# Performance work log

Measured on AMD Instinct MI355X. Metric: run time of the kernel, lower is better.

The kernel has to match this reference:

```python
import jax, jax.numpy as jnp
import numpy as np

# --- static config (matches init_kwargs) ---
B, N, FD, Y, X = 2, 4, 128, 64, 64   # batch, n_views, feat_dim, H, W
DIM, HEADS, DH = 128, 4, 128          # dim, heads, dim_head (= dim)
INNER = HEADS * DH                    # 512
BN = B * N
EPS = 1e-5


def _ln(x, g, b):
    # LayerNorm over last dim, eps=1e-5, affine
    m = x.mean(-1, keepdims=True)
    v = ((x - m) ** 2).mean(-1, keepdims=True)
    return (x - m) * jax.lax.rsqrt(v + EPS) * g + b


def _inorm(x):
    # InstanceNorm2d (no affine): normalize each (sample, channel) over H,W
    m = x.mean((2, 3), keepdims=True)
    v = ((x - m) ** 2).mean((2, 3), keepdims=True)
    return (x - m) * jax.lax.rsqrt(v + EPS)


def _conv2x2_s2(x, w):
    # Conv2d(k=2, stride=2, no bias): non-overlapping windows -> einsum
    b, c, h, wd = x.shape
    xp = x.reshape(b, c, h // 2, 2, wd // 2, 2)
    return jnp.einsum('bchawd,ocad->bohw', xp, w)


def _convT2x2_s2(x, w):
    # ConvTranspose2d(k=2, stride=2, no bias); w in torch layout (I, O, 2, 2)
    b, i, h, wd = x.shape
    y = jnp.einsum('bihw,ioad->bohawd', x, w)
    return y.reshape(b, w.shape[1], 2 * h, 2 * wd)


def _forward(cam_feat, lidar_feat, pos_embed, conv_w, convT_w,
             lnq_g, lnq_b, wq, lnk_g, lnk_b, wk, lnv_g, lnv_b, wv,
             proj_w, proj_b, pre_g, pre_b,
             mlp_w1, mlp_b1, mlp_w2, mlp_b2, post_g, post_b):
    h, w = Y // 2, X // 2
    bev = pos_embed[None, None]                      # (1,1,FD,Y,X)
    cam = (cam_feat + bev).reshape(BN, FD, Y, X)
    lid = (lidar_feat + bev).reshape(BN, FD, Y, X)
    cam_e = _conv2x2_s2(jax.nn.relu(_inorm(cam)), conv_w)   # (BN,DIM,h,w)
    lid_e = _conv2x2_s2(jax.nn.relu(_inorm(lid)), conv_w)

    cam_flat = cam_e.reshape(BN, DIM, h * w)
    lid_flat = lid_e.reshape(BN, DIM, h * w)
    # query = cat([cam, lidar]) along token axis -> (BN, 2hw, DIM)
    q_in = jnp.concatenate([cam_flat, lid_flat], -1).transpose(0, 2, 1)
    # skip = cat([cam_embed, lidar_embed]) along width -> 'b d H W -> b (H W) d'
    skip = jnp.concatenate([cam_e, lid_e], -1).transpose(0, 2, 3, 1).reshape(BN, 2 * h * w, DIM)

    def cross(kv_flat):
        k_in = kv_flat.transpose(0, 2, 1)            # (BN, hw, DIM)
        q = (_ln(q_in, lnq_g, lnq_b) @ wq).reshape(BN, -1, HEADS, DH)
        k = (_ln(k_in, lnk_g, lnk_b) @ wk).reshape(BN, -1, HEADS, DH)
        v = (_ln(k_in, lnv_g, lnv_b) @ wv).reshape(BN, -1, HEADS, DH)
        dot = jnp.einsum('bqhd,bkhd->bhqk', q, k) * (DH ** -0.5)
        att = jax.nn.softmax(dot, axis=-1)
        a = jnp.einsum('bhqk,bkhd->bqhd', att, v).reshape(BN, -1, INNER)
        z = a @ proj_w + proj_b + skip
        z = _ln(z, pre_g, pre_b)
        z = z + (jax.nn.gelu(z @ mlp_w1 + mlp_b1, approximate=False) @ mlp_w2 + mlp_b2)
        z = _ln(z, post_g, post_b)
        # '(b l) (H W) d -> b l d H W' with H=Y, W=X//2
        return z.reshape(B, N, Y, X // 2, DIM).transpose(0, 1, 4, 2, 3)

    cam_fused = cross(cam_flat)                      # (B,N,DIM,Y,X//2)
    lid_fused = cross(lid_flat)
    fused = cam_fused + lid_fused
    # 'b l d (m h) w -> b l d h w m' then sum over m=2
    fused = fused.reshape(B, N, DIM, 2, Y // 2, X // 2).sum(3)
    fused_feat = _convT2x2_s2(jax.nn.relu(_inorm(fused.reshape(BN, DIM, Y // 2, X // 2))), convT_w)
    cam_out = _convT2x2_s2(jax.nn.relu(_inorm(cam_fused.reshape(BN, DIM, Y, X // 2))), convT_w)
    lid_out = _convT2x2_s2(jax.nn.relu(_inorm(lid_fused.reshape(BN, DIM, Y, X // 2))), convT_w)
    return fused_feat, cam_out, lid_out


def setup_inputs() -> dict:
    key = jax.random.key(0)
    ks = jax.random.split(key, 12)
    f = lambda k, shape, s=0.02: (jax.random.normal(k, shape, jnp.float32) * s)
    return {
        'cam_feat': jax.random.normal(ks[0], (B, N, FD, Y, X), jnp.float32),
        'lidar_feat': jax.random.normal(ks[1], (B, N, FD, Y, X), jnp.float32),
        'pos_embed': jax.random.normal(ks[2], (FD, Y, X), jnp.float32),
        'conv_w': f(ks[3], (DIM, FD, 2, 2), 0.05),
        'convT_w': f(ks[4], (DIM, FD, 2, 2), 0.05),
        'lnq_g': jnp.ones(DIM), 'lnq_b': jnp.zeros(DIM), 'wq': f(ks[5], (DIM, INNER)),
        'lnk_g': jnp.ones(DIM), 'lnk_b': jnp.zeros(DIM), 'wk': f(ks[6], (DIM, INNER)),
        'lnv_g': jnp.ones(DIM), 'lnv_b': jnp.zeros(DIM), 'wv': f(ks[7], (DIM, INNER)),
        'proj_w': f(ks[8], (INNER, DIM)), 'proj_b': jnp.zeros(DIM),
        'pre_g': jnp.ones(DIM), 'pre_b': jnp.zeros(DIM),
        'mlp_w1': f(ks[9], (DIM, 2 * DIM)), 'mlp_b1': jnp.zeros(2 * DIM),
        'mlp_w2': f(ks[10], (2 * DIM, DIM)), 'mlp_b2': jnp.zeros(DIM),
        'post_g': jnp.ones(DIM), 'post_b': jnp.zeros(DIM),
    }


def reference(cam_feat, lidar_feat, pos_embed, conv_w, convT_w,
              lnq_g, lnq_b, wq, lnk_g, lnk_b, wk, lnv_g, lnv_b, wv,
              proj_w, proj_b, pre_g, pre_b,
              mlp_w1, mlp_b1, mlp_w2, mlp_b2, post_g, post_b):
    return _forward(cam_feat, lidar_feat, pos_embed, conv_w, convT_w,
                    lnq_g, lnq_b, wq, lnk_g, lnk_b, wk, lnv_g, lnv_b, wv,
                    proj_w, proj_b, pre_g, pre_b,
                    mlp_w1, mlp_b1, mlp_w2, mlp_b2, post_g, post_b)
```

## Files before the change

kernel.cpp:

```cpp
#include <hip/hip_runtime.h>
#include <math.h>

#define TPB 256

typedef __attribute__((ext_vector_type(8))) short bf16x8;
typedef __attribute__((ext_vector_type(4))) float f32x4;

__device__ __forceinline__ float gelu_exact(float x) {
    return 0.5f * x * (1.0f + erff(x * 0.70710678118654752f));
}

__device__ __forceinline__ unsigned short f2bf(float x) {
    unsigned u = __float_as_uint(x);
    return (unsigned short)((u + 0x7fffu + ((u >> 16) & 1u)) >> 16);
}

__global__ void k_stats_cm(const float* __restrict__ x0, const float* __restrict__ x1,
                           const float* __restrict__ pos, float* __restrict__ mean,
                           float* __restrict__ rstd) {
    int gc = blockIdx.x;
    const float* src = ((gc < 1024) ? x0 : x1) + (size_t)(gc & 1023) * 4096;
    const float* posr = pos + (size_t)(gc & 127) * 4096;
    float s = 0.f, s2 = 0.f;
    for (int p = threadIdx.x; p < 4096; p += TPB) {
        float v = src[p] + posr[p];
        s += v; s2 += v * v;
    }
#pragma unroll
    for (int m = 32; m; m >>= 1) { s += __shfl_xor(s, m); s2 += __shfl_xor(s2, m); }
    __shared__ float ls[4], ls2[4];
    int w = threadIdx.x >> 6;
    if ((threadIdx.x & 63) == 0) { ls[w] = s; ls2[w] = s2; }
    __syncthreads();
    if (threadIdx.x == 0) {
        s = ls[0] + ls[1] + ls[2] + ls[3];
        s2 = ls2[0] + ls2[1] + ls2[2] + ls2[3];
        float mu = s / 4096.f;
        float var = s2 / 4096.f - mu * mu;
        mean[gc] = mu;
        rstd[gc] = rsqrtf(var + 1e-5f);
    }
}

__global__ void k_stats_red(const float* __restrict__ part, float* __restrict__ mean,
                            float* __restrict__ rstd, int nc, int T) {
    int b = blockIdx.x, d = threadIdx.x;
    float s = 0.f, s2 = 0.f;
    for (int c = 0; c < nc; c++) {
        const float* p = part + ((size_t)(b * nc + c) * 2) * 128;
        s += p[d]; s2 += p[128 + d];
    }
    float mu = s / (float)T;
    float var = s2 / (float)T - mu * mu;
    mean[b * 128 + d] = mu;
    rstd[b * 128 + d] = rsqrtf(var + 1e-5f);
}

__global__ void k_stats_red2(const float* __restrict__ part,
                             float* __restrict__ meanC, float* __restrict__ rstdC,
                             float* __restrict__ meanL, float* __restrict__ rstdL) {
    int idx = blockIdx.x, d = threadIdx.x;
    int sel = idx >> 3, b = idx & 7;
    float s = 0.f, s2 = 0.f;
    for (int c = 0; c < 32; c++) {
        const float* p = part + ((size_t)((sel * 8 + b) * 32 + c) * 2) * 128;
        s += p[d]; s2 += p[128 + d];
    }
    float mu = s / 2048.f;
    float var = s2 / 2048.f - mu * mu;
    float* mean = sel ? meanL : meanC;
    float* rstd = sel ? rstdL : rstdC;
    mean[b * 128 + d] = mu;
    rstd[b * 128 + d] = rsqrtf(var + 1e-5f);
}

__global__ void k_prep(const float* __restrict__ cam, const float* __restrict__ lid,
                       const float* __restrict__ pos, const float* __restrict__ mean,
                       const float* __restrict__ rstd, unsigned short* __restrict__ xcolT) {
    __shared__ unsigned short T[32 * 520];
    int h = blockIdx.x, bb = blockIdx.y;
    int b = bb & 7, so = (bb < 8) ? 0 : 1024;
    const float* x = (bb < 8) ? cam : lid;
    int tid = threadIdx.x;
    for (int i = tid; i < 4096; i += TPB) {
        int c = i >> 5, w = i & 31;
        int ch = b * 128 + c;
        const float* xr = x + (size_t)ch * 4096 + (2 * h) * 64 + 2 * w;
        const float* pr = pos + (size_t)c * 4096 + (2 * h) * 64 + 2 * w;
        float mu = mean[so + ch], rs = rstd[so + ch];
        float2 x0 = *(const float2*)xr;
        float2 x1 = *(const float2*)(xr + 64);
        float2 p0 = *(const float2*)pr;
        float2 p1 = *(const float2*)(pr + 64);
        ushort4 u;
        u.x = f2bf(fmaxf((x0.x + p0.x - mu) * rs, 0.f));
        u.y = f2bf(fmaxf((x0.y + p0.y - mu) * rs, 0.f));
        u.z = f2bf(fmaxf((x1.x + p1.x - mu) * rs, 0.f));
        u.w = f2bf(fmaxf((x1.y + p1.y - mu) * rs, 0.f));
        *(ushort4*)&T[w * 520 + c * 4] = u;
    }
    __syncthreads();
    unsigned short* dst = xcolT + ((size_t)bb * 1024 + h * 32) * 512;
    for (int i = tid; i < 2048; i += TPB) {
        int w = i >> 6, kk = (i & 63) * 8;
        *(bf16x8*)&dst[(size_t)w * 512 + kk] = *(bf16x8*)&T[w * 520 + kk];
    }
}

__global__ __launch_bounds__(256, 2) void k_conv_gemm(
        const float* __restrict__ W, const unsigned short* __restrict__ xcolT,
        float* __restrict__ camT, float* __restrict__ lidT,
        float* __restrict__ mean_e, float* __restrict__ rstd_e) {
    __shared__ __align__(16) unsigned short As[128 * 40];
    __shared__ __align__(16) unsigned short Bs[64 * 40];
    __shared__ float red[2048];
    int tid = threadIdx.x, lane = tid & 63, w = tid >> 6;
    int l16 = lane & 15, lhi = lane >> 4;
    int n0 = blockIdx.x * 64, bb = blockIdx.z;
    const unsigned short* BT = xcolT + (size_t)bb * 524288;
    float* eT = ((bb < 8) ? camT : lidT) + (size_t)(bb & 7) * 131072;

    f32x4 acc[2][4];
#pragma unroll
    for (int mi = 0; mi < 2; mi++)
#pragma unroll
        for (int ni = 0; ni < 4; ni++) acc[mi][ni] = (f32x4){0.f, 0.f, 0.f, 0.f};

    for (int k0 = 0; k0 < 512; k0 += 32) {
        for (int i = tid; i < 1024; i += TPB) {
            int row = i >> 3, kc = (i & 7) * 4;
            float4 va = *(const float4*)&W[(size_t)row * 512 + k0 + kc];
            ushort4 u;
            u.x = f2bf(va.x); u.y = f2bf(va.y); u.z = f2bf(va.z); u.w = f2bf(va.w);
            *(ushort4*)&As[row * 40 + kc] = u;
        }
        for (int i = tid; i < 256; i += TPB) {
            int n = i >> 2, kc = (i & 3) * 8;
            *(bf16x8*)&Bs[n * 40 + kc] = *(const bf16x8*)&BT[(size_t)(n0 + n) * 512 + k0 + kc];
        }
        __syncthreads();
        bf16x8 af[2], bfr[4];
#pragma unroll
        for (int mi = 0; mi < 2; mi++)
            af[mi] = *(bf16x8*)&As[(w * 32 + mi * 16 + l16) * 40 + lhi * 8];
#pragma unroll
        for (int ni = 0; ni < 4; ni++)
            bfr[ni] = *(bf16x8*)&Bs[(ni * 16 + l16) * 40 + lhi * 8];
#pragma unroll
        for (int mi = 0; mi < 2; mi++)
#pragma unroll
            for (int ni = 0; ni < 4; ni++)
                acc[mi][ni] = __builtin_amdgcn_mfma_f32_16x16x32_bf16(af[mi], bfr[ni], acc[mi][ni], 0, 0, 0);
        __syncthreads();
    }
#pragma unroll
    for (int mi = 0; mi < 2; mi++)
#pragma unroll
        for (int ni = 0; ni < 4; ni++) {
            int col = n0 + ni * 16 + l16;
            int rowb = w * 32 + mi * 16 + lhi * 4;
            *(float4*)&eT[(size_t)col * 128 + rowb] = *(float4*)&acc[mi][ni];
        }
#pragma unroll
    for (int ni = 0; ni < 4; ni++) {
        float s = 0.f, s2 = 0.f;
#pragma unroll
        for (int mi = 0; mi < 2; mi++)
#pragma unroll
            for (int rg = 0; rg < 4; rg++) {
                float v = acc[mi][ni][rg];
                s += v; s2 += v * v;
            }
        int idx = (ni * 16 + l16) * 16 + w * 4 + lhi;
        red[idx] = s;
        red[1024 + idx] = s2;
    }
    __syncthreads();
    if (tid < 64) {
        int ni = tid >> 4, c16 = tid & 15;
        float s = 0.f, s2 = 0.f;
#pragma unroll
        for (int j = 0; j < 16; j++) {
            s += red[(ni * 16 + c16) * 16 + j];
            s2 += red[1024 + (ni * 16 + c16) * 16 + j];
        }
        int col = n0 + ni * 16 + c16;
        int tok = bb * 1024 + col;
        float mu = s * (1.f / 128.f);
        float var = s2 * (1.f / 128.f) - mu * mu;
        mean_e[tok] = mu;
        rstd_e[tok] = rsqrtf(var + 1e-5f);
    }
}

__global__ void k_wtrans_all(
        const float* __restrict__ wq, const float* __restrict__ wk,
        const float* __restrict__ wv, const float* __restrict__ proj,
        const float* __restrict__ m1, const float* __restrict__ m2,
        const float* __restrict__ ct,
        const float* __restrict__ gq, const float* __restrict__ gk,
        const float* __restrict__ gv,
        const float* __restrict__ bq_in, const float* __restrict__ bk_in,
        const float* __restrict__ bv_in,
        unsigned short* wqT, unsigned short* wkT, unsigned short* wvT,
        unsigned short* projT, unsigned short* m1T, unsigned short* m2T,
        unsigned short* ctT, float* __restrict__ bout) {
    __shared__ float t[32][33];
    int bid = blockIdx.x;
    int tid = threadIdx.x;
    if (bid >= 384) {
        int i = bid - 384;
        int which = i >> 1, half = i & 1;
        const float* W = (which == 0) ? wq : (which == 1) ? wk : wv;
        const float* bb = (which == 0) ? bq_in : (which == 1) ? bk_in : bv_in;
        int n = half * 256 + tid;
        float s = 0.f;
        for (int k = 0; k < 128; k++) s += bb[k] * W[(size_t)k * 512 + n];
        bout[which * 512 + n] = s;
        return;
    }
    const float* W; unsigned short* WT; const float* sc = nullptr; int K, N, ti;
    if (bid < 64)       { W = wq;   WT = wqT;   sc = gq; K = 128; N = 512; ti = bid; }
    else if (bid < 128) { W = wk;   WT = wkT;   sc = gk; K = 128; N = 512; ti = bid - 64; }
    else if (bid < 192) { W = wv;   WT = wvT;   sc = gv; K = 128; N = 512; ti = bid - 128; }
    else if (bid < 256) { W = proj; WT = projT; K = 512; N = 128; ti = bid - 192; }
    else if (bid < 288) { W = m1;   WT = m1T;   K = 128; N = 256; ti = bid - 256; }
    else if (bid < 320) { W = m2;   WT = m2T;   K = 256; N = 128; ti = bid - 288; }
    else                { W = ct;   WT = ctT;   K = 128; N = 512; ti = bid - 320; }
    int tx = N >> 5;
    int n0 = (ti % tx) * 32, k0 = (ti / tx) * 32;
    for (int i = tid; i < 1024; i += TPB) {
        int r = i >> 5, c = i & 31;
        float v = W[(size_t)(k0 + r) * N + n0 + c];
        if (sc) v *= sc[k0 + r];
        t[r][c] = v;
    }
    __syncthreads();
    for (int i = tid; i < 1024; i += TPB) {
        int r = i >> 5, c = i & 31;
        WT[(size_t)(n0 + r) * K + k0 + c] = f2bf(t[c][r]);
    }
}

__global__ __launch_bounds__(256, 2) void k_qkv_gemm(
        const float* __restrict__ camT, const float* __restrict__ lidT,
        const float* __restrict__ me, const float* __restrict__ re,
        const unsigned short* __restrict__ wqT, const unsigned short* __restrict__ wkT,
        const unsigned short* __restrict__ wvT,
        unsigned short* __restrict__ qout, unsigned short* __restrict__ kout,
        unsigned short* __restrict__ vout,
        const float* __restrict__ bvecs, float qscale) {
    __shared__ __align__(16) unsigned short As[128 * 40];
    __shared__ __align__(16) unsigned short Bs[128 * 40];
    int tid = threadIdx.x, lane = tid & 63, w = tid >> 6;
    int l16 = lane & 15, lhi = lane >> 4;
    int wm = w >> 1, wn = w & 1;
    int which = blockIdx.x >> 2;
    int n0 = (blockIdx.x & 3) * 128;
    int m0 = blockIdx.y * 128;
    const unsigned short* BT = (which == 0) ? wqT : (which == 1) ? wkT : wvT;
    const float* bias = bvecs + which * 512;

    f32x4 acc[4][4];
#pragma unroll
    for (int mi = 0; mi < 4; mi++)
#pragma unroll
        for (int ni = 0; ni < 4; ni++) acc[mi][ni] = (f32x4){0.f, 0.f, 0.f, 0.f};

    for (int k0 = 0; k0 < 128; k0 += 32) {
        for (int i = tid; i < 1024; i += TPB) {
            int row = i >> 3, kc = (i & 7) * 4;
            int r = m0 + row;
            const float* srow;
            int tok;
            if (which == 0) {
                int b = r >> 11, t = r & 2047;
                bool cam = t < 1024;
                tok = (cam ? b : 8 + b) * 1024 + (t & 1023);
                srow = (cam ? camT : lidT) + (size_t)(b * 1024 + (t & 1023)) * 128;
            } else {
                tok = r;
                srow = ((r < 8192) ? camT : lidT) + (size_t)(r & 8191) * 128;
            }
            float mu = me[tok], rs = re[tok];
            float4 va = *(const float4*)&srow[k0 + kc];
            ushort4 u;
            u.x = f2bf((va.x - mu) * rs); u.y = f2bf((va.y - mu) * rs);
            u.z = f2bf((va.z - mu) * rs); u.w = f2bf((va.w - mu) * rs);
            *(ushort4*)&As[row * 40 + kc] = u;
        }
        for (int i = tid; i < 512; i += TPB) {
            int n = i >> 2, kc = (i & 3) * 8;
            *(bf16x8*)&Bs[n * 40 + kc] = *(const bf16x8*)&BT[(size_t)(n0 + n) * 128 + k0 + kc];
        }
        __syncthreads();
        bf16x8 af[4], bfr[4];
#pragma unroll
        for (int mi = 0; mi < 4; mi++)
            af[mi] = *(bf16x8*)&As[(wm * 64 + mi * 16 + l16) * 40 + lhi * 8];
#pragma unroll
        for (int ni = 0; ni < 4; ni++)
            bfr[ni] = *(bf16x8*)&Bs[(wn * 64 + ni * 16 + l16) * 40 + lhi * 8];
#pragma unroll
        for (int mi = 0; mi < 4; mi++)
#pragma unroll
            for (int ni = 0; ni < 4; ni++)
                acc[mi][ni] = __builtin_amdgcn_mfma_f32_16x16x32_bf16(af[mi], bfr[ni], acc[mi][ni], 0, 0, 0);
        __syncthreads();
    }
#pragma unroll
    for (int mi = 0; mi < 4; mi++) {
#pragma unroll
        for (int ni = 0; ni < 4; ni++) {
            int col = n0 + wn * 64 + ni * 16 + l16;
            float bc = bias[col];
            if (which == 2) {
                int row0 = m0 + wm * 64 + mi * 16 + lhi * 4;
                int bb = row0 >> 10, t0 = row0 & 1023;
                ushort4 u;
                u.x = f2bf(acc[mi][ni][0] + bc); u.y = f2bf(acc[mi][ni][1] + bc);
                u.z = f2bf(acc[mi][ni][2] + bc); u.w = f2bf(acc[mi][ni][3] + bc);
                *(ushort4*)&vout[(((size_t)(bb * 4 + (col >> 7))) * 128 + (col & 127)) * 1024 + t0] = u;
            } else {
                int sT = (which == 0) ? 11 : 10;
                float sc = (which == 0) ? qscale : 1.f;
                unsigned short* C16 = (which == 0) ? qout : kout;
#pragma unroll
                for (int rg = 0; rg < 4; rg++) {
                    int row = m0 + wm * 64 + mi * 16 + lhi * 4 + rg;
                    int bb = row >> sT, t = row & ((1 << sT) - 1);
                    size_t oa = ((((size_t)bb * 4 + (col >> 7)) << sT) + t) * 128 + (col & 127);
                    C16[oa] = f2bf((acc[mi][ni][rg] + bc) * sc);
                }
            }
        }
    }
}

__global__ __launch_bounds__(256, 2) void k_gemm_gelu(
        const float* __restrict__ A, const unsigned short* __restrict__ BT,
        unsigned short* __restrict__ C16, int N, int K,
        const float* __restrict__ bias) {
    __shared__ __align__(16) unsigned short As[128 * 40];
    __shared__ __align__(16) unsigned short Bs[128 * 40];
    int tid = threadIdx.x, lane = tid & 63, w = tid >> 6;
    int l16 = lane & 15, lhi = lane >> 4;
    int wm = w >> 1, wn = w & 1;
    int m0 = blockIdx.y * 128, n0 = blockIdx.x * 128;

    f32x4 acc[4][4];
#pragma unroll
    for (int mi = 0; mi < 4; mi++)
#pragma unroll
        for (int ni = 0; ni < 4; ni++) acc[mi][ni] = (f32x4){0.f, 0.f, 0.f, 0.f};

    for (int k0 = 0; k0 < K; k0 += 32) {
        for (int i = tid; i < 1024; i += TPB) {
            int row = i >> 3, kc = (i & 7) * 4;
            float4 va = *(const float4*)&A[(size_t)(m0 + row) * K + k0 + kc];
            ushort4 u;
            u.x = f2bf(va.x); u.y = f2bf(va.y); u.z = f2bf(va.z); u.w = f2bf(va.w);
            *(ushort4*)&As[row * 40 + kc] = u;
        }
        for (int i = tid; i < 512; i += TPB) {
            int n = i >> 2, kc = (i & 3) * 8;
            *(bf16x8*)&Bs[n * 40 + kc] = *(const bf16x8*)&BT[(size_t)(n0 + n) * K + k0 + kc];
        }
        __syncthreads();
        bf16x8 af[4], bfr[4];
#pragma unroll
        for (int mi = 0; mi < 4; mi++)
            af[mi] = *(bf16x8*)&As[(wm * 64 + mi * 16 + l16) * 40 + lhi * 8];
#pragma unroll
        for (int ni = 0; ni < 4; ni++)
            bfr[ni] = *(bf16x8*)&Bs[(wn * 64 + ni * 16 + l16) * 40 + lhi * 8];
#pragma unroll
        for (int mi = 0; mi < 4; mi++)
#pragma unroll
            for (int ni = 0; ni < 4; ni++)
                acc[mi][ni] = __builtin_amdgcn_mfma_f32_16x16x32_bf16(af[mi], bfr[ni], acc[mi][ni], 0, 0, 0);
        __syncthreads();
    }
#pragma unroll
    for (int mi = 0; mi < 4; mi++)
#pragma unroll
        for (int ni = 0; ni < 4; ni++) {
            int col = n0 + wn * 64 + ni * 16 + l16;
            float bc = bias[col];
#pragma unroll
            for (int rg = 0; rg < 4; rg++) {
                int row = m0 + wm * 64 + mi * 16 + lhi * 4 + rg;
                C16[(size_t)row * N + col] = f2bf(gelu_exact(acc[mi][ni][rg] + bc));
            }
        }
}

__global__ __launch_bounds__(256, 2) void k_gemm_ln(
        const unsigned short* __restrict__ Ab, const unsigned short* __restrict__ BT,
        float* __restrict__ C0, float* __restrict__ C1, int K, int mode,
        const float* __restrict__ bias, const float* __restrict__ aux,
        const float* __restrict__ aux2,
        const float* __restrict__ g, const float* __restrict__ bvec,
        float* __restrict__ part) {
    __shared__ __align__(16) char shm[64 * 132 * 4];
    unsigned short* As = (unsigned short*)shm;
    unsigned short* Bs = As + 64 * 40;
    float* Cs = (float*)shm;
    int tid = threadIdx.x, lane = tid & 63, w = tid >> 6;
    int l16 = lane & 15, lhi = lane >> 4;
    int m0 = blockIdx.x * 64;

    f32x4 acc[4][2];
#pragma unroll
    for (int mi = 0; mi < 4; mi++)
#pragma unroll
        for (int ni = 0; ni < 2; ni++) acc[mi][ni] = (f32x4){0.f, 0.f, 0.f, 0.f};

    for (int k0 = 0; k0 < K; k0 += 32) {
        for (int i = tid; i < 256; i += TPB) {
            int row = i >> 2, kc = (i & 3) * 8;
            *(bf16x8*)&As[row * 40 + kc] =
                *(const bf16x8*)&Ab[(size_t)(m0 + row) * K + k0 + kc];
        }
        for (int i = tid; i < 512; i += TPB) {
            int n = i >> 2, kc = (i & 3) * 8;
            *(bf16x8*)&Bs[n * 40 + kc] = *(const bf16x8*)&BT[(size_t)n * K + k0 + kc];
        }
        __syncthreads();
        bf16x8 af[4], bfr[2];
#pragma unroll
        for (int mi = 0; mi < 4; mi++)
            af[mi] = *(bf16x8*)&As[(mi * 16 + l16) * 40 + lhi * 8];
#pragma unroll
        for (int ni = 0; ni < 2; ni++)
            bfr[ni] = *(bf16x8*)&Bs[(w * 32 + ni * 16 + l16) * 40 + lhi * 8];
#pragma unroll
        for (int mi = 0; mi < 4; mi++)
#pragma unroll
            for (int ni = 0; ni < 2; ni++)
                acc[mi][ni] = __builtin_amdgcn_mfma_f32_16x16x32_bf16(af[mi], bfr[ni], acc[mi][ni], 0, 0, 0);
        __syncthreads();
    }
#pragma unroll
    for (int mi = 0; mi < 4; mi++) {
#pragma unroll
        for (int ni = 0; ni < 2; ni++) {
            int col = w * 32 + ni * 16 + l16;
#pragma unroll
            for (int rg = 0; rg < 4; rg++) {
                int rl = mi * 16 + lhi * 4 + rg;
                int grow = m0 + rl;
                float v = acc[mi][ni][rg] + bias[col];
                if (mode == 0) {
                    int rr = grow & 16383;
                    int b = rr >> 11, s = rr & 2047;
                    int H = s >> 6, W = s & 63;
                    const float* sp = (W < 32) ? aux : aux2;
                    v += sp[((size_t)(b * 1024 + H * 32 + (W & 31))) * 128 + col];
                } else {
                    v += aux[(size_t)grow * 128 + col];
                }
                Cs[rl * 132 + col] = v;
            }
        }
    }
    __syncthreads();
    float sl = 0.f, sl2 = 0.f, sh = 0.f, sh2 = 0.f;
    for (int rr = 0; rr < 16; rr++) {
        int row = w * 16 + rr, grow = m0 + row;
        float x0 = Cs[row * 132 + lane], x1 = Cs[row * 132 + 64 + lane];
        float s = x0 + x1, s2 = x0 * x0 + x1 * x1;
#pragma unroll
        for (int m = 32; m; m >>= 1) { s += __shfl_xor(s, m); s2 += __shfl_xor(s2, m); }
        float mu = s * (1.f / 128.f);
        float var = s2 * (1.f / 128.f) - mu * mu;
        float rs = rsqrtf(var + 1e-5f);
        float o0 = (x0 - mu) * rs * g[lane] + bvec[lane];
        float o1 = (x1 - mu) * rs * g[lane + 64] + bvec[lane + 64];
        float* Cp;
        size_t ro;
        if (mode == 1) { Cp = (grow < 16384) ? C0 : C1; ro = (size_t)(grow & 16383) * 128; }
        else           { Cp = C0; ro = (size_t)grow * 128; }
        Cp[ro + lane]      = o0;
        Cp[ro + lane + 64] = o1;
        sl += o0; sl2 += o0 * o0; sh += o1; sh2 += o1 * o1;
    }
    if (mode == 1) {
        __syncthreads();
        float* redS = Cs;
        redS[w * 128 + lane] = sl;
        redS[w * 128 + 64 + lane] = sh;
        redS[512 + w * 128 + lane] = sl2;
        redS[512 + w * 128 + 64 + lane] = sh2;
        __syncthreads();
        if (tid < 128) {
            int d = tid;
            float S = 0.f, S2 = 0.f;
#pragma unroll
            for (int j = 0; j < 4; j++) {
                S += redS[j * 128 + d];
                S2 += redS[512 + j * 128 + d];
            }
            int sel = (m0 >= 16384) ? 1 : 0;
            int rrg = m0 & 16383;
            int b = rrg >> 11, c = (rrg >> 6) & 31;
            float* p = part + ((size_t)((sel * 8 + b) * 32 + c) * 2) * 128;
            p[d] = S; p[128 + d] = S2;
        }
    }
}

__global__ __launch_bounds__(256, 2) void k_convt_gemm(
        const float* __restrict__ srcF, const float* __restrict__ srcC,
        const float* __restrict__ srcL, const float* __restrict__ stats,
        const unsigned short* __restrict__ ctT, float* __restrict__ outp) {
    __shared__ __align__(16) unsigned short As[128 * 40];
    __shared__ __align__(16) unsigned short Bs[128 * 40];
    int tid = threadIdx.x, lane = tid & 63, w = tid >> 6;
    int l16 = lane & 15, lhi = lane >> 4;
    int wm = w >> 1, wn = w & 1;
    int my = blockIdx.y, n0 = blockIdx.x * 128, b = blockIdx.z;
    const float* src; const float* mean; const float* rstd; float* out;
    int M, Hin, m0;
    if (my < 8)       { src = srcF; mean = stats + 4096; rstd = stats + 5120;
                        out = outp;            M = 1024; Hin = 32; m0 = my * 128; }
    else if (my < 24) { src = srcC; mean = stats + 6144; rstd = stats + 7168;
                        out = outp + 4194304;  M = 2048; Hin = 64; m0 = (my - 8) * 128; }
    else              { src = srcL; mean = stats + 8192; rstd = stats + 9216;
                        out = outp + 12582912; M = 2048; Hin = 64; m0 = (my - 24) * 128; }
    const float* Ab = src + (size_t)b * M * 128;
    const float* mb = mean + b * 128;
    const float* rb = rstd + b * 128;

    f32x4 acc[4][4];
#pragma unroll
    for (int mi = 0; mi < 4; mi++)
#pragma unroll
        for (int ni = 0; ni < 4; ni++) acc[mi][ni] = (f32x4){0.f, 0.f, 0.f, 0.f};

    for (int k0 = 0; k0 < 128; k0 += 32) {
        for (int i = tid; i < 1024; i += TPB) {
            int row = i >> 3, kc = (i & 7) * 4;
            float4 va = *(const float4*)&Ab[(size_t)(m0 + row) * 128 + k0 + kc];
            float4 mn = *(const float4*)&mb[k0 + kc];
            float4 rs = *(const float4*)&rb[k0 + kc];
            ushort4 u;
            u.x = f2bf(fmaxf((va.x - mn.x) * rs.x, 0.f));
            u.y = f2bf(fmaxf((va.y - mn.y) * rs.y, 0.f));
            u.z = f2bf(fmaxf((va.z - mn.z) * rs.z, 0.f));
            u.w = f2bf(fmaxf((va.w - mn.w) * rs.w, 0.f));
            *(ushort4*)&As[row * 40 + kc] = u;
        }
        for (int i = tid; i < 512; i += TPB) {
            int n = i >> 2, kc = (i & 3) * 8;
            *(bf16x8*)&Bs[n * 40 + kc] = *(const bf16x8*)&ctT[(size_t)(n0 + n) * 128 + k0 + kc];
        }
        __syncthreads();
        bf16x8 af[4], bfr[4];
#pragma unroll
        for (int mi = 0; mi < 4; mi++)
            af[mi] = *(bf16x8*)&As[(wm * 64 + mi * 16 + l16) * 40 + lhi * 8];
#pragma unroll
        for (int ni = 0; ni < 4; ni++)
            bfr[ni] = *(bf16x8*)&Bs[(wn * 64 + ni * 16 + l16) * 40 + lhi * 8];
#pragma unroll
        for (int mi = 0; mi < 4; mi++)
#pragma unroll
            for (int ni = 0; ni < 4; ni++)
                acc[mi][ni] = __builtin_amdgcn_mfma_f32_16x16x32_bf16(af[mi], bfr[ni], acc[mi][ni], 0, 0, 0);
        __syncthreads();
    }
    int Ho = 2 * Hin, Wo = 64;
#pragma unroll
    for (int mi = 0; mi < 4; mi++) {
#pragma unroll
        for (int ni = 0; ni < 4; ni++) {
            int col = n0 + wn * 64 + ni * 16 + l16;
            int oc = col >> 2, aa = (col >> 1) & 1, dd = col & 1;
            int p0 = m0 + wm * 64 + mi * 16 + lhi * 4;
            int hin = p0 >> 5, win0 = p0 & 31;
            float s0 = __shfl_xor(acc[mi][ni][0], 1);
            float s1 = __shfl_xor(acc[mi][ni][1], 1);
            float s2 = __shfl_xor(acc[mi][ni][2], 1);
            float s3 = __shfl_xor(acc[mi][ni][3], 1);
            float4 o;
            if (!dd) o = make_float4(acc[mi][ni][0], s0, acc[mi][ni][1], s1);
            else     o = make_float4(s2, acc[mi][ni][2], s3, acc[mi][ni][3]);
            size_t addr = (((size_t)b * 128 + oc) * Ho + 2 * hin + aa) * Wo
                        + 2 * win0 + (dd ? 4 : 0);
            *(float4*)&out[addr] = o;
        }
    }
}

__global__ __launch_bounds__(256, 2) void k_attn_bf16(
        const unsigned short* __restrict__ qb, const unsigned short* __restrict__ kb,
        const unsigned short* __restrict__ vt, unsigned short* __restrict__ aout) {
    __shared__ __align__(16) unsigned short smem[24576];
    unsigned short* Ks = smem;
    unsigned short* Vt = smem + 8192;
    unsigned short* Ps = smem + 16384;
    int tid = threadIdx.x;
    int lane = tid & 63, w = tid >> 6;
    int l16 = lane & 15, lhi = lane >> 4;
    int bid = blockIdx.x;
    int xcd = bid & 7, j = bid >> 3;
    int hz = xcd * 8 + (j >> 4);
    int qt = j & 15;
    int h = hz & 3, z = hz >> 2;
    int bh_q = (z & 7) * 4 + h;
    int bh_kv = z * 4 + h;
    unsigned short* Pw = Ps + w * 2048;

    const unsigned short* qg = qb + ((size_t)bh_q * 2048 + qt * 128) * 128;
    bf16x8 qa[2][4];
#pragma unroll
    for (int mt = 0; mt < 2; mt++) {
        int r = w * 32 + mt * 16 + l16;
#pragma unroll
        for (int ks = 0; ks < 4; ks++)
            qa[mt][ks] = *(const bf16x8*)&qg[(size_t)r * 128 + ks * 32 + lhi * 8];
    }

    f32x4 acc[2][8];
#pragma unroll
    for (int mt = 0; mt < 2; mt++)
#pragma unroll
        for (int dt = 0; dt < 8; dt++) acc[mt][dt] = (f32x4){0.f, 0.f, 0.f, 0.f};
    float m_r[2] = {-1e30f, -1e30f};
    float l_r[2] = {0.f, 0.f};

    const unsigned short* kg = kb + (size_t)bh_kv * 131072;
    const unsigned short* vg = vt + (size_t)bh_kv * 131072;

    int krow = tid >> 4, kcol = (tid & 15) * 8;
    int kls = ((tid & 15) ^ (krow & 7)) << 3;
    int vrow = tid >> 3, vcol = (tid & 7) * 8;
    int vls = ((tid & 7) ^ (vrow & 7)) << 3;

#pragma unroll
    for (int jj = 0; jj < 4; jj++) {
        int r = krow + jj * 16;
        *(bf16x8*)&Ks[r * 128 + kls] = *(const bf16x8*)&kg[(size_t)r * 128 + kcol];
        int d = vrow + jj * 32;
        *(bf16x8*)&Vt[d * 64 + vls] = *(const bf16x8*)&vg[(size_t)d * 1024 + vcol];
    }
    __syncthreads();

    for (int c = 0; c < 16; c++) {
        bf16x8 kpre[4], vpre[4];
        if (c < 15) {
            int c0 = (c + 1) * 64;
#pragma unroll
            for (int jj = 0; jj < 4; jj++) {
                kpre[jj] = *(const bf16x8*)&kg[(size_t)(c0 + krow + jj * 16) * 128 + kcol];
                vpre[jj] = *(const bf16x8*)&vg[(size_t)(vrow + jj * 32) * 1024 + c0 + vcol];
            }
        }

        f32x4 s[2][4];
#pragma unroll
        for (int mt = 0; mt < 2; mt++)
#pragma unroll
            for (int kt = 0; kt < 4; kt++) s[mt][kt] = (f32x4){0.f, 0.f, 0.f, 0.f};
        __builtin_amdgcn_s_setprio(1);
#pragma unroll
        for (int kt = 0; kt < 4; kt++) {
            int r = kt * 16 + l16;
#pragma unroll
            for (int ks = 0; ks < 4; ks++) {
                bf16x8 kf = *(bf16x8*)&Ks[r * 128 + (((ks * 4 + lhi) ^ (r & 7)) << 3)];
                s[0][kt] = __builtin_amdgcn_mfma_f32_16x16x32_bf16(kf, qa[0][ks], s[0][kt], 0, 0, 0);
                s[1][kt] = __builtin_amdgcn_mfma_f32_16x16x32_bf16(kf, qa[1][ks], s[1][kt], 0, 0, 0);
            }
        }
        __builtin_amdgcn_s_setprio(0);

        float pm[2];
#pragma unroll
        for (int mt = 0; mt < 2; mt++) {
            float a = s[mt][0][0];
#pragma unroll
            for (int kt = 0; kt < 4; kt++)
#pragma unroll
                for (int rg = 0; rg < 4; rg++) a = fmaxf(a, s[mt][kt][rg]);
            a = fmaxf(a, __shfl_xor(a, 16));
            a = fmaxf(a, __shfl_xor(a, 32));
            pm[mt] = a;
        }
        bool need = (pm[0] > m_r[0] + 8.f) || (pm[1] > m_r[1] + 8.f);
        if (__any(need)) {
#pragma unroll
            for (int mt = 0; mt < 2; mt++) {
                float mn = fmaxf(m_r[mt], pm[mt]);
                float f = __builtin_amdgcn_exp2f(m_r[mt] - mn);
                m_r[mt] = mn;
                l_r[mt] *= f;
#pragma unroll
                for (int rg = 0; rg < 4; rg++) {
                    float ft = __shfl(f, lhi * 4 + rg);
#pragma unroll
                    for (int dt = 0; dt < 8; dt++) acc[mt][dt][rg] *= ft;
                }
            }
        }

#pragma unroll
        for (int mt = 0; mt < 2; mt++) {
            int row = mt * 16 + l16;
            int rsw = row & 7;
            float ls = 0.f;
#pragma unroll
            for (int kt = 0; kt < 4; kt++) {
                float p0 = __builtin_amdgcn_exp2f(s[mt][kt][0] - m_r[mt]);
                float p1 = __builtin_amdgcn_exp2f(s[mt][kt][1] - m_r[mt]);
                float p2 = __builtin_amdgcn_exp2f(s[mt][kt][2] - m_r[mt]);
                float p3 = __builtin_amdgcn_exp2f(s[mt][kt][3] - m_r[mt]);
                ls += (p0 + p1) + (p2 + p3);
                unsigned u01, u23;
                asm("v_cvt_pk_bf16_f32 %0, %1, %2" : "=v"(u01) : "v"(p0), "v"(p1));
                asm("v_cvt_pk_bf16_f32 %0, %1, %2" : "=v"(u23) : "v"(p2), "v"(p3));
                int slot = kt * 2 + (lhi >> 1);
                int base = row * 64 + ((slot ^ rsw) << 3) + (lhi & 1) * 4;
                *(unsigned*)&Pw[base] = u01;
                *(unsigned*)&Pw[base + 2] = u23;
            }
            l_r[mt] += ls;
        }
        asm volatile("s_waitcnt lgkmcnt(0)" ::: "memory");

        bf16x8 pa0[2], pa1[2];
#pragma unroll
        for (int mt = 0; mt < 2; mt++) {
            int row = mt * 16 + l16;
            pa0[mt] = *(bf16x8*)&Pw[row * 64 + ((lhi ^ (row & 7)) << 3)];
            pa1[mt] = *(bf16x8*)&Pw[row * 64 + (((4 + lhi) ^ (row & 7)) << 3)];
        }
        __builtin_amdgcn_s_setprio(1);
#pragma unroll
        for (int dt = 0; dt < 8; dt++) {
            int d = dt * 16 + l16;
            bf16x8 vb0 = *(bf16x8*)&Vt[d * 64 + ((lhi ^ (d & 7)) << 3)];
            bf16x8 vb1 = *(bf16x8*)&Vt[d * 64 + (((4 + lhi) ^ (d & 7)) << 3)];
            acc[0][dt] = __builtin_amdgcn_mfma_f32_16x16x32_bf16(pa0[0], vb0, acc[0][dt], 0, 0, 0);
            acc[0][dt] = __builtin_amdgcn_mfma_f32_16x16x32_bf16(pa1[0], vb1, acc[0][dt], 0, 0, 0);
            acc[1][dt] = __builtin_amdgcn_mfma_f32_16x16x32_bf16(pa0[1], vb0, acc[1][dt], 0, 0, 0);
            acc[1][dt] = __builtin_amdgcn_mfma_f32_16x16x32_bf16(pa1[1], vb1, acc[1][dt], 0, 0, 0);
        }
        __builtin_amdgcn_s_setprio(0);
        __syncthreads();

        if (c < 15) {
#pragma unroll
            for (int jj = 0; jj < 4; jj++) {
                *(bf16x8*)&Ks[(krow + jj * 16) * 128 + kls] = kpre[jj];
                *(bf16x8*)&Vt[(vrow + jj * 32) * 64 + vls] = vpre[jj];
            }
            __syncthreads();
        }
    }

#pragma unroll
    for (int mt = 0; mt < 2; mt++) {
        float lt = l_r[mt];
        lt += __shfl_xor(lt, 16);
        lt += __shfl_xor(lt, 32);
        l_r[mt] = lt;
    }
    size_t obase = (size_t)(z >> 3) * 16384 + (size_t)(z & 7) * 2048;
#pragma unroll
    for (int mt = 0; mt < 2; mt++)
#pragma unroll
        for (int rg = 0; rg < 4; rg++) {
            float linv = 1.f / __shfl(l_r[mt], lhi * 4 + rg);
            int qrow = qt * 128 + w * 32 + mt * 16 + lhi * 4 + rg;
            unsigned short* orow = aout + (obase + qrow) * 512 + h * 128;
#pragma unroll
            for (int dt = 0; dt < 8; dt++)
                orow[dt * 16 + l16] = f2bf(acc[mt][dt][rg] * linv);
        }
}

__global__ void k_fused_stats(const float* __restrict__ zc, const float* __restrict__ zl,
                              float* __restrict__ fs, float* __restrict__ part) {
    int c = blockIdx.x, b = blockIdx.y;
    int tid = threadIdx.x;
    int d = tid & 127, half = tid >> 7;
    size_t base0 = ((size_t)b * 2048 + c * 64) * 128;
    size_t base1 = ((size_t)b * 2048 + 1024 + c * 64) * 128;
    float s = 0.f, s2 = 0.f;
    for (int t = half; t < 64; t += 2) {
        float v = zc[base0 + t * 128 + d] + zc[base1 + t * 128 + d]
                + zl[base0 + t * 128 + d] + zl[base1 + t * 128 + d];
        fs[((size_t)b * 1024 + c * 64 + t) * 128 + d] = v;
        s += v; s2 += v * v;
    }
    __shared__ float ls[256], ls2[256];
    ls[tid] = s; ls2[tid] = s2;
    __syncthreads();
    if (tid < 128) {
        s = ls[tid] + ls[tid + 128];
        s2 = ls2[tid] + ls2[tid + 128];
        float* p = part + ((size_t)(b * 16 + c) * 2) * 128;
        p[d] = s; p[128 + d] = s2;
    }
}

extern "C" void kernel_launch(void* const* d_in, const int* in_sizes, int n_in,
                              void* d_out, int out_size, void* d_ws, size_t ws_size,
                              hipStream_t stream) {
    const float* cam_feat = (const float*)d_in[0];
    const float* lid_feat = (const float*)d_in[1];
    const float* pos      = (const float*)d_in[2];
    const float* conv_w   = (const float*)d_in[3];
    const float* convT_w  = (const float*)d_in[4];
    const float* lnq_g = (const float*)d_in[5];
    const float* lnq_b = (const float*)d_in[6];
    const float* wq    = (const float*)d_in[7];
    const float* lnk_g = (const float*)d_in[8];
    const float* lnk_b = (const float*)d_in[9];
    const float* wk    = (const float*)d_in[10];
    const float* lnv_g = (const float*)d_in[11];
    const float* lnv_b = (const float*)d_in[12];
    const float* wv    = (const float*)d_in[13];
    const float* proj_w = (const float*)d_in[14];
    const float* proj_b = (const float*)d_in[15];
    const float* pre_g = (const float*)d_in[16];
    const float* pre_b = (const float*)d_in[17];
    const float* mlp_w1 = (const float*)d_in[18];
    const float* mlp_b1 = (const float*)d_in[19];
    const float* mlp_w2 = (const float*)d_in[20];
    const float* mlp_b2 = (const float*)d_in[21];
    const float* post_g = (const float*)d_in[22];
    const float* post_b = (const float*)d_in[23];

    float* ws = (float*)d_ws;
    float* outp = (float*)d_out;

    float* cam_eT  = ws + 0;
    float* lid_eT  = ws + 1048576;
    unsigned short* qbf16 = (unsigned short*)(ws + 2097152);
    float* z_cam   = ws + 6291456;
    float* z_lid   = ws + 8388608;
    float* fused_s = ws + 10485760;
    float* stats   = ws + 11534336;
    unsigned short* wbuf = (unsigned short*)(ws + 11550720);
    float* part    = ws + 11747328;
    float* mean_e  = ws + 11878400;
    float* rstd_e  = ws + 11894784;
    float* bvecs   = ws + 11911168;
    unsigned short* xcolT = (unsigned short*)(ws + 11912704);
    float* pool    = ws + 16107008;

    unsigned short* wqT   = wbuf + 0;
    unsigned short* wkT   = wbuf + 65536;
    unsigned short* wvT   = wbuf + 131072;
    unsigned short* projT = wbuf + 196608;
    unsigned short* m1T   = wbuf + 262144;
    unsigned short* m2T   = wbuf + 294912;
    unsigned short* ctT   = wbuf + 327680;

    float* meanA = stats + 0,    *rstdA = stats + 2048;
    float* meanF = stats + 4096, *rstdF = stats + 5120;

    unsigned short* kbf16 = (unsigned short*)(pool + 0);
    unsigned short* vbfT  = (unsigned short*)(pool + 4194304);
    unsigned short* abuf  = (unsigned short*)(pool + 8388608);
    float* z2 = pool + 0;
    unsigned short* h1 = (unsigned short*)(pool + 4194304);

    const float qscale = 0.12751744436f;

    k_wtrans_all<<<390, TPB, 0, stream>>>(wq, wk, wv, proj_w, mlp_w1, mlp_w2, convT_w,
                                          lnq_g, lnk_g, lnv_g, lnq_b, lnk_b, lnv_b,
                                          wqT, wkT, wvT, projT, m1T, m2T, ctT, bvecs);

    k_stats_cm<<<2048, TPB, 0, stream>>>(cam_feat, lid_feat, pos, meanA, rstdA);
    k_prep<<<dim3(32, 16), TPB, 0, stream>>>(cam_feat, lid_feat, pos, meanA, rstdA, xcolT);
    k_conv_gemm<<<dim3(16, 1, 16), TPB, 0, stream>>>(conv_w, xcolT, cam_eT, lid_eT,
                                                     mean_e, rstd_e);

    k_qkv_gemm<<<dim3(12, 128), TPB, 0, stream>>>(
        cam_eT, lid_eT, mean_e, rstd_e, wqT, wkT, wvT, qbf16, kbf16, vbfT,
        bvecs, qscale);
    k_attn_bf16<<<1024, TPB, 0, stream>>>(qbf16, kbf16, vbfT, abuf);
    k_gemm_ln<<<512, TPB, 0, stream>>>(
        abuf, projT, z2, nullptr, 512, 0, proj_b, cam_eT, lid_eT, pre_g, pre_b, nullptr);
    k_gemm_gelu<<<dim3(2, 256), TPB, 0, stream>>>(z2, m1T, h1, 256, 128, mlp_b1);
    k_gemm_ln<<<512, TPB, 0, stream>>>(
        h1, m2T, z_cam, z_lid, 256, 1, mlp_b2, z2, nullptr, post_g, post_b, part);

    k_stats_red2<<<16, 128, 0, stream>>>(part, stats + 6144, stats + 7168,
                                         stats + 8192, stats + 9216);
    k_fused_stats<<<dim3(16, 8), TPB, 0, stream>>>(z_cam, z_lid, fused_s, part + 65536);
    k_stats_red<<<8, 128, 0, stream>>>(part + 65536, meanF, rstdF, 16, 1024);
    k_convt_gemm<<<dim3(4, 40, 8), TPB, 0, stream>>>(fused_s, z_cam, z_lid, stats,
                                                     ctT, outp);
}
```

Measured before the change: 298.2 us.

## Fuse projection, pre-LN, MLP and post-LN into one per-token-tile kernel

Replaces three kernels (proj GEMM+LN, MLP1 GEMM+GELU, MLP2 GEMM+LN) with a single kernel that keeps each 64-token tile's intermediates in registers and swizzled LDS. Computing the transposed product lets each lane own one token's full row, so LayerNorm needs only a few shuffles. This removes the global round-trips for z2 and h1 and two launches. In exchange the MLP weights are re-streamed per block and register pressure is higher, which may reduce occupancy.

```diff
diff --git a/kernel.cpp b/kernel.cpp
--- a/kernel.cpp
+++ b/kernel.cpp
@@ -337,176 +337,203 @@
     }
 }
 
-__global__ __launch_bounds__(256, 2) void k_gemm_gelu(
-        const float* __restrict__ A, const unsigned short* __restrict__ BT,
-        unsigned short* __restrict__ C16, int N, int K,
-        const float* __restrict__ bias) {
-    __shared__ __align__(16) unsigned short As[128 * 40];
-    __shared__ __align__(16) unsigned short Bs[128 * 40];
-    int tid = threadIdx.x, lane = tid & 63, w = tid >> 6;
-    int l16 = lane & 15, lhi = lane >> 4;
-    int wm = w >> 1, wn = w & 1;
-    int m0 = blockIdx.y * 128, n0 = blockIdx.x * 128;
-
-    f32x4 acc[4][4];
-#pragma unroll
-    for (int mi = 0; mi < 4; mi++)
-#pragma unroll
-        for (int ni = 0; ni < 4; ni++) acc[mi][ni] = (f32x4){0.f, 0.f, 0.f, 0.f};
-
-    for (int k0 = 0; k0 < K; k0 += 32) {
-        for (int i = tid; i < 1024; i += TPB) {
-            int row = i >> 3, kc = (i & 7) * 4;
-            float4 va = *(const float4*)&A[(size_t)(m0 + row) * K + k0 + kc];
-            ushort4 u;
-            u.x = f2bf(va.x); u.y = f2bf(va.y); u.z = f2bf(va.z); u.w = f2bf(va.w);
-            *(ushort4*)&As[row * 40 + kc] = u;
-        }
-        for (int i = tid; i < 512; i += TPB) {
-            int n = i >> 2, kc = (i & 3) * 8;
-            *(bf16x8*)&Bs[n * 40 + kc] = *(const bf16x8*)&BT[(size_t)(n0 + n) * K + k0 + kc];
-        }
-        __syncthreads();
-        bf16x8 af[4], bfr[4];
-#pragma unroll
-        for (int mi = 0; mi < 4; mi++)
-            af[mi] = *(bf16x8*)&As[(wm * 64 + mi * 16 + l16) * 40 + lhi * 8];
-#pragma unroll
-        for (int ni = 0; ni < 4; ni++)
-            bfr[ni] = *(bf16x8*)&Bs[(wn * 64 + ni * 16 + l16) * 40 + lhi * 8];
-#pragma unroll
-        for (int mi = 0; mi < 4; mi++)
-#pragma unroll
-            for (int ni = 0; ni < 4; ni++)
-                acc[mi][ni] = __builtin_amdgcn_mfma_f32_16x16x32_bf16(af[mi], bfr[ni], acc[mi][ni], 0, 0, 0);
-        __syncthreads();
-    }
-#pragma unroll
-    for (int mi = 0; mi < 4; mi++)
-#pragma unroll
-        for (int ni = 0; ni < 4; ni++) {
-            int col = n0 + wn * 64 + ni * 16 + l16;
-            float bc = bias[col];
-#pragma unroll
-            for (int rg = 0; rg < 4; rg++) {
-                int row = m0 + wm * 64 + mi * 16 + lhi * 4 + rg;
-                C16[(size_t)row * N + col] = f2bf(gelu_exact(acc[mi][ni][rg] + bc));
-            }
-        }
-}
-
-__global__ __launch_bounds__(256, 2) void k_gemm_ln(
-        const unsigned short* __restrict__ Ab, const unsigned short* __restrict__ BT,
-        float* __restrict__ C0, float* __restrict__ C1, int K, int mode,
-        const float* __restrict__ bias, const float* __restrict__ aux,
-        const float* __restrict__ aux2,
-        const float* __restrict__ g, const float* __restrict__ bvec,
+__global__ __launch_bounds__(256, 2) void k_tail_fused(
+        const unsigned short* __restrict__ abuf, const unsigned short* __restrict__ projT,
+        const unsigned short* __restrict__ m1T, const unsigned short* __restrict__ m2T,
+        const float* __restrict__ camT, const float* __restrict__ lidT,
+        const float* __restrict__ proj_b,
+        const float* __restrict__ pre_g, const float* __restrict__ pre_b,
+        const float* __restrict__ mlp_b1, const float* __restrict__ mlp_b2,
+        const float* __restrict__ post_g, const float* __restrict__ post_b,
+        float* __restrict__ z_cam, float* __restrict__ z_lid,
         float* __restrict__ part) {
-    __shared__ __align__(16) char shm[64 * 132 * 4];
-    unsigned short* As = (unsigned short*)shm;
-    unsigned short* Bs = As + 64 * 40;
-    float* Cs = (float*)shm;
+    __shared__ __align__(16) unsigned short shm[21504];
     int tid = threadIdx.x, lane = tid & 63, w = tid >> 6;
     int l16 = lane & 15, lhi = lane >> 4;
     int m0 = blockIdx.x * 64;
-
-    f32x4 acc[4][2];
-#pragma unroll
-    for (int mi = 0; mi < 4; mi++)
-#pragma unroll
-        for (int ni = 0; ni < 2; ni++) acc[mi][ni] = (f32x4){0.f, 0.f, 0.f, 0.f};
-
-    for (int k0 = 0; k0 < K; k0 += 32) {
+    int tok = w * 16 + l16;
+    int grow = m0 + tok;
+    int tsw = tok & 7;
+
+    unsigned short* Ts = shm;
+    unsigned short* Ws = shm + 2560;
+    f32x4 z2[8];
+#pragma unroll
+    for (int ni = 0; ni < 8; ni++) z2[ni] = (f32x4){0.f, 0.f, 0.f, 0.f};
+    for (int k0 = 0; k0 < 512; k0 += 32) {
         for (int i = tid; i < 256; i += TPB) {
             int row = i >> 2, kc = (i & 3) * 8;
-            *(bf16x8*)&As[row * 40 + kc] =
-                *(const bf16x8*)&Ab[(size_t)(m0 + row) * K + k0 + kc];
+            *(bf16x8*)&Ts[row * 40 + kc] =
+                *(const bf16x8*)&abuf[(size_t)(m0 + row) * 512 + k0 + kc];
         }
         for (int i = tid; i < 512; i += TPB) {
-            int n = i >> 2, kc = (i & 3) * 8;
-            *(bf16x8*)&Bs[n * 40 + kc] = *(const bf16x8*)&BT[(size_t)n * K + k0 + kc];
-        }
-        __syncthreads();
-        bf16x8 af[4], bfr[2];
-#pragma unroll
-        for (int mi = 0; mi < 4; mi++)
-            af[mi] = *(bf16x8*)&As[(mi * 16 + l16) * 40 + lhi * 8];
-#pragma unroll
-        for (int ni = 0; ni < 2; ni++)
-            bfr[ni] = *(bf16x8*)&Bs[(w * 32 + ni * 16 + l16) * 40 + lhi * 8];
-#pragma unroll
-        for (int mi = 0; mi < 4; mi++)
-#pragma unroll
-            for (int ni = 0; ni < 2; ni++)
-                acc[mi][ni] = __builtin_amdgcn_mfma_f32_16x16x32_bf16(af[mi], bfr[ni], acc[mi][ni], 0, 0, 0);
-        __syncthreads();
-    }
-#pragma unroll
-    for (int mi = 0; mi < 4; mi++) {
-#pragma unroll
-        for (int ni = 0; ni < 2; ni++) {
-            int col = w * 32 + ni * 16 + l16;
-#pragma unroll
-            for (int rg = 0; rg < 4; rg++) {
-                int rl = mi * 16 + lhi * 4 + rg;
-                int grow = m0 + rl;
-                float v = acc[mi][ni][rg] + bias[col];
-                if (mode == 0) {
-                    int rr = grow & 16383;
-                    int b = rr >> 11, s = rr & 2047;
-                    int H = s >> 6, W = s & 63;
-                    const float* sp = (W < 32) ? aux : aux2;
-                    v += sp[((size_t)(b * 1024 + H * 32 + (W & 31))) * 128 + col];
-                } else {
-                    v += aux[(size_t)grow * 128 + col];
-                }
-                Cs[rl * 132 + col] = v;
-            }
-        }
-    }
-    __syncthreads();
-    float sl = 0.f, sl2 = 0.f, sh = 0.f, sh2 = 0.f;
-    for (int rr = 0; rr < 16; rr++) {
-        int row = w * 16 + rr, grow = m0 + row;
-        float x0 = Cs[row * 132 + lane], x1 = Cs[row * 132 + 64 + lane];
-        float s = x0 + x1, s2 = x0 * x0 + x1 * x1;
-#pragma unroll
-        for (int m = 32; m; m >>= 1) { s += __shfl_xor(s, m); s2 += __shfl_xor(s2, m); }
+            int row = i >> 2, kc = (i & 3) * 8;
+            *(bf16x8*)&Ws[row * 40 + kc] =
+                *(const bf16x8*)&projT[(size_t)row * 512 + k0 + kc];
+        }
+        __syncthreads();
+        bf16x8 bfr = *(bf16x8*)&Ts[tok * 40 + lhi * 8];
+#pragma unroll
+        for (int ni = 0; ni < 8; ni++) {
+            bf16x8 af = *(bf16x8*)&Ws[(ni * 16 + l16) * 40 + lhi * 8];
+            z2[ni] = __builtin_amdgcn_mfma_f32_16x16x32_bf16(af, bfr, z2[ni], 0, 0, 0);
+        }
+        __syncthreads();
+    }
+    {
+        int rr = grow & 16383;
+        int b = rr >> 11, ss = rr & 2047;
+        int Hh = ss >> 6, Ww = ss & 63;
+        const float* sp = ((Ww < 32) ? camT : lidT)
+                        + ((size_t)(b * 1024 + Hh * 32 + (Ww & 31))) * 128;
+#pragma unroll
+        for (int ni = 0; ni < 8; ni++) {
+            int c0 = ni * 16 + lhi * 4;
+            float4 pb = *(const float4*)&proj_b[c0];
+            float4 sk = *(const float4*)&sp[c0];
+            z2[ni][0] += pb.x + sk.x; z2[ni][1] += pb.y + sk.y;
+            z2[ni][2] += pb.z + sk.z; z2[ni][3] += pb.w + sk.w;
+        }
+    }
+    unsigned short* z2ln = shm;
+    {
+        float s = 0.f, s2 = 0.f;
+#pragma unroll
+        for (int ni = 0; ni < 8; ni++)
+#pragma unroll
+            for (int rg = 0; rg < 4; rg++) { float v = z2[ni][rg]; s += v; s2 += v * v; }
+        s += __shfl_xor(s, 16); s2 += __shfl_xor(s2, 16);
+        s += __shfl_xor(s, 32); s2 += __shfl_xor(s2, 32);
         float mu = s * (1.f / 128.f);
         float var = s2 * (1.f / 128.f) - mu * mu;
         float rs = rsqrtf(var + 1e-5f);
-        float o0 = (x0 - mu) * rs * g[lane] + bvec[lane];
-        float o1 = (x1 - mu) * rs * g[lane + 64] + bvec[lane + 64];
-        float* Cp;
-        size_t ro;
-        if (mode == 1) { Cp = (grow < 16384) ? C0 : C1; ro = (size_t)(grow & 16383) * 128; }
-        else           { Cp = C0; ro = (size_t)grow * 128; }
-        Cp[ro + lane]      = o0;
-        Cp[ro + lane + 64] = o1;
-        sl += o0; sl2 += o0 * o0; sh += o1; sh2 += o1 * o1;
-    }
-    if (mode == 1) {
-        __syncthreads();
-        float* redS = Cs;
-        redS[w * 128 + lane] = sl;
-        redS[w * 128 + 64 + lane] = sh;
-        redS[512 + w * 128 + lane] = sl2;
-        redS[512 + w * 128 + 64 + lane] = sh2;
-        __syncthreads();
-        if (tid < 128) {
-            int d = tid;
-            float S = 0.f, S2 = 0.f;
-#pragma unroll
-            for (int j = 0; j < 4; j++) {
-                S += redS[j * 128 + d];
-                S2 += redS[512 + j * 128 + d];
-            }
-            int sel = (m0 >= 16384) ? 1 : 0;
-            int rrg = m0 & 16383;
-            int b = rrg >> 11, c = (rrg >> 6) & 31;
-            float* p = part + ((size_t)((sel * 8 + b) * 32 + c) * 2) * 128;
-            p[d] = S; p[128 + d] = S2;
-        }
+#pragma unroll
+        for (int ni = 0; ni < 8; ni++) {
+            int c0 = ni * 16 + lhi * 4;
+            float4 gg = *(const float4*)&pre_g[c0];
+            float4 bb = *(const float4*)&pre_b[c0];
+            z2[ni][0] = (z2[ni][0] - mu) * rs * gg.x + bb.x;
+            z2[ni][1] = (z2[ni][1] - mu) * rs * gg.y + bb.y;
+            z2[ni][2] = (z2[ni][2] - mu) * rs * gg.z + bb.z;
+            z2[ni][3] = (z2[ni][3] - mu) * rs * gg.w + bb.w;
+            unsigned u01, u23;
+            asm("v_cvt_pk_bf16_f32 %0, %1, %2" : "=v"(u01) : "v"(z2[ni][0]), "v"(z2[ni][1]));
+            asm("v_cvt_pk_bf16_f32 %0, %1, %2" : "=v"(u23) : "v"(z2[ni][2]), "v"(z2[ni][3]));
+            int slot = ni * 2 + (lhi >> 1);
+            int base = tok * 128 + ((slot ^ tsw) << 3) + (lhi & 1) * 4;
+            *(unsigned*)&z2ln[base] = u01;
+            *(unsigned*)&z2ln[base + 2] = u23;
+        }
+    }
+
+    unsigned short* As1 = shm + 8192;
+    f32x4 a1[16];
+#pragma unroll
+    for (int ni = 0; ni < 16; ni++) a1[ni] = (f32x4){0.f, 0.f, 0.f, 0.f};
+    for (int ks = 0; ks < 4; ks++) {
+        int k0 = ks * 32;
+        for (int i = tid; i < 1024; i += TPB) {
+            int row = i >> 2, kc = (i & 3) * 8;
+            *(bf16x8*)&As1[row * 40 + kc] =
+                *(const bf16x8*)&m1T[(size_t)row * 128 + k0 + kc];
+        }
+        __syncthreads();
+        bf16x8 bfr = *(bf16x8*)&z2ln[tok * 128 + (((ks * 4 + lhi) ^ tsw) << 3)];
+#pragma unroll
+        for (int ni = 0; ni < 16; ni++) {
+            bf16x8 af = *(bf16x8*)&As1[(ni * 16 + l16) * 40 + lhi * 8];
+            a1[ni] = __builtin_amdgcn_mfma_f32_16x16x32_bf16(af, bfr, a1[ni], 0, 0, 0);
+        }
+        __syncthreads();
+    }
+    unsigned short* Hs = shm;
+#pragma unroll
+    for (int ni = 0; ni < 16; ni++) {
+        int c0 = ni * 16 + lhi * 4;
+        float4 bb = *(const float4*)&mlp_b1[c0];
+        float h0 = gelu_exact(a1[ni][0] + bb.x);
+        float h1v = gelu_exact(a1[ni][1] + bb.y);
+        float h2 = gelu_exact(a1[ni][2] + bb.z);
+        float h3 = gelu_exact(a1[ni][3] + bb.w);
+        unsigned u01, u23;
+        asm("v_cvt_pk_bf16_f32 %0, %1, %2" : "=v"(u01) : "v"(h0), "v"(h1v));
+        asm("v_cvt_pk_bf16_f32 %0, %1, %2" : "=v"(u23) : "v"(h2), "v"(h3));
+        int slot = ni * 2 + (lhi >> 1);
+        int base = tok * 256 + ((slot ^ tsw) << 3) + (lhi & 1) * 4;
+        *(unsigned*)&Hs[base] = u01;
+        *(unsigned*)&Hs[base + 2] = u23;
+    }
+
+    unsigned short* As2 = shm + 16384;
+    f32x4 a2[8];
+#pragma unroll
+    for (int ni = 0; ni < 8; ni++) a2[ni] = (f32x4){0.f, 0.f, 0.f, 0.f};
+    for (int ks = 0; ks < 8; ks++) {
+        int k0 = ks * 32;
+        for (int i = tid; i < 512; i += TPB) {
+            int row = i >> 2, kc = (i & 3) * 8;
+            *(bf16x8*)&As2[row * 40 + kc] =
+                *(const bf16x8*)&m2T[(size_t)row * 256 + k0 + kc];
+        }
+        __syncthreads();
+        bf16x8 bfr = *(bf16x8*)&Hs[tok * 256 + (((ks * 4 + lhi) ^ tsw) << 3)];
+#pragma unroll
+        for (int ni = 0; ni < 8; ni++) {
+            bf16x8 af = *(bf16x8*)&As2[(ni * 16 + l16) * 40 + lhi * 8];
+            a2[ni] = __builtin_amdgcn_mfma_f32_16x16x32_bf16(af, bfr, a2[ni], 0, 0, 0);
+        }
+        __syncthreads();
+    }
+    float* O = (float*)shm;
+    {
+#pragma unroll
+        for (int ni = 0; ni < 8; ni++) {
+            int c0 = ni * 16 + lhi * 4;
+            float4 bb = *(const float4*)&mlp_b2[c0];
+            a2[ni][0] += bb.x + z2[ni][0];
+            a2[ni][1] += bb.y + z2[ni][1];
+            a2[ni][2] += bb.z + z2[ni][2];
+            a2[ni][3] += bb.w + z2[ni][3];
+        }
+        float s = 0.f, s2 = 0.f;
+#pragma unroll
+        for (int ni = 0; ni < 8; ni++)
+#pragma unroll
+            for (int rg = 0; rg < 4; rg++) { float v = a2[ni][rg]; s += v; s2 += v * v; }
+        s += __shfl_xor(s, 16); s2 += __shfl_xor(s2, 16);
+        s += __shfl_xor(s, 32); s2 += __shfl_xor(s2, 32);
+        float mu = s * (1.f / 128.f);
+        float var = s2 * (1.f / 128.f) - mu * mu;
+        float rs = rsqrtf(var + 1e-5f);
+        float* Cp = (grow < 16384) ? z_cam : z_lid;
+        size_t ro = (size_t)(grow & 16383) * 128;
+#pragma unroll
+        for (int ni = 0; ni < 8; ni++) {
+            int c0 = ni * 16 + lhi * 4;
+            float4 gg = *(const float4*)&post_g[c0];
+            float4 bb = *(const float4*)&post_b[c0];
+            float4 o;
+            o.x = (a2[ni][0] - mu) * rs * gg.x + bb.x;
+            o.y = (a2[ni][1] - mu) * rs * gg.y + bb.y;
+            o.z = (a2[ni][2] - mu) * rs * gg.z + bb.z;
+            o.w = (a2[ni][3] - mu) * rs * gg.w + bb.w;
+            *(float4*)&Cp[ro + c0] = o;
+            *(float4*)&O[tok * 132 + c0] = o;
+        }
+    }
+    __syncthreads();
+    if (tid < 128) {
+        int col = tid;
+        float s = 0.f, s2 = 0.f;
+        for (int t = 0; t < 64; t++) {
+            float v = O[t * 132 + col];
+            s += v; s2 += v * v;
+        }
+        int sel = (m0 >= 16384) ? 1 : 0;
+        int rrg = m0 & 16383;
+        int b = rrg >> 11, c = (rrg >> 6) & 31;
+        float* p = part + ((size_t)((sel * 8 + b) * 32 + c) * 2) * 128;
+        p[col] = s; p[128 + col] = s2;
     }
 }
 
@@ -866,8 +893,6 @@
     unsigned short* kbf16 = (unsigned short*)(pool + 0);
     unsigned short* vbfT  = (unsigned short*)(pool + 4194304);
     unsigned short* abuf  = (unsigned short*)(pool + 8388608);
-    float* z2 = pool + 0;
-    unsigned short* h1 = (unsigned short*)(pool + 4194304);
 
     const float qscale = 0.12751744436f;
 
@@ -884,11 +909,9 @@
         cam_eT, lid_eT, mean_e, rstd_e, wqT, wkT, wvT, qbf16, kbf16, vbfT,
         bvecs, qscale);
     k_attn_bf16<<<1024, TPB, 0, stream>>>(qbf16, kbf16, vbfT, abuf);
-    k_gemm_ln<<<512, TPB, 0, stream>>>(
-        abuf, projT, z2, nullptr, 512, 0, proj_b, cam_eT, lid_eT, pre_g, pre_b, nullptr);
-    k_gemm_gelu<<<dim3(2, 256), TPB, 0, stream>>>(z2, m1T, h1, 256, 128, mlp_b1);
-    k_gemm_ln<<<512, TPB, 0, stream>>>(
-        h1, m2T, z_cam, z_lid, 256, 1, mlp_b2, z2, nullptr, post_g, post_b, part);
+    k_tail_fused<<<512, TPB, 0, stream>>>(
+        abuf, projT, m1T, m2T, cam_eT, lid_eT, proj_b, pre_g, pre_b,
+        mlp_b1, mlp_b2, post_g, post_b, z_cam, z_lid, part);
 
     k_stats_red2<<<16, 128, 0, stream>>>(part, stats + 6144, stats + 7168,
                                          stats + 8192, stats + 9216);
```

New measurement: 267.7 us. -10.2%, faster.
